# Performance work log

Measured on AMD Instinct MI355X. Metric: run time of the kernel, lower is better.

Reference implementation:

```python
import jax, jax.numpy as jnp
import numpy as np

BATCH = 16384
IN_F = 4096
OUT_F = 4096
CP_H = 4
CP_W = 4
CP_B = 4


def _cubic_interp_matrix(n_out: int, n_cp: int, a: float = -0.75) -> jnp.ndarray:
    """Dense (n_out, n_cp) matrix replicating torch bicubic interpolation
    (Keys cubic convolution, a=-0.75) along one axis with align_corners=True
    and border replication (index clamping)."""
    # source coordinate for each output index (align_corners=True)
    x = jnp.arange(n_out, dtype=jnp.float32) * ((n_cp - 1) / (n_out - 1))
    x0 = jnp.floor(x)
    t = x - x0                      # fractional offset in [0,1)
    x0i = x0.astype(jnp.int32)

    def cub_inner(s):   # |s| <= 1
        return ((a + 2.0) * s - (a + 3.0)) * s * s + 1.0

    def cub_outer(s):   # 1 < |s| < 2
        return ((a * s - 5.0 * a) * s + 8.0 * a) * s - 4.0 * a

    # weights for taps at offsets -1, 0, +1, +2
    ws = (cub_outer(t + 1.0), cub_inner(t), cub_inner(1.0 - t), cub_outer(2.0 - t))
    A = jnp.zeros((n_out, n_cp), dtype=jnp.float32)
    for k, w in enumerate(ws):
        idx = jnp.clip(x0i + (k - 1), 0, n_cp - 1)  # replicate border
        A = A + w[:, None] * jax.nn.one_hot(idx, n_cp, dtype=jnp.float32)
    return A


def _linear_interp_matrix(n_out: int, n_cp: int) -> jnp.ndarray:
    """Dense (n_out, n_cp) matrix replicating torch 1-D linear interpolation
    with align_corners=True."""
    x = jnp.arange(n_out, dtype=jnp.float32) * ((n_cp - 1) / (n_out - 1))
    lo = jnp.floor(x).astype(jnp.int32)
    t = x - lo.astype(jnp.float32)
    hi = jnp.clip(lo + 1, 0, n_cp - 1)
    oh = lambda i: jax.nn.one_hot(i, n_cp, dtype=jnp.float32)
    return (1.0 - t)[:, None] * oh(lo) + t[:, None] * oh(hi)


def setup_inputs() -> dict:
    key = jax.random.key(0)
    k1, k2, k3 = jax.random.split(key, 3)
    return {
        "x": jax.random.normal(k1, (BATCH, IN_F), dtype=jnp.float32),
        "weight_cp": jax.random.normal(k2, (CP_H, CP_W), dtype=jnp.float32) * 0.02,
        "bias_cp": jax.random.normal(k3, (CP_B,), dtype=jnp.float32) * 0.02,
    }


def reference(x, weight_cp, bias_cp):
    # Bicubic-interpolated dense weight: W = A_out @ CP @ A_in^T  (out, in)
    A_out = _cubic_interp_matrix(OUT_F, CP_H)
    A_in = _cubic_interp_matrix(IN_F, CP_W)
    W = A_out @ weight_cp @ A_in.T
    # Linearly interpolated bias (out,)
    bias = _linear_interp_matrix(OUT_F, CP_B) @ bias_cp
    # F.linear: y = x @ W^T + b
    return x @ W.T + bias
```

## Files before the change

kernel.cpp:

```cpp
#include <hip/hip_runtime.h>
#include <cstddef>

#define BATCH 16384
#define IN_F  4096
#define OUT_F 4096
#define ROWS_PER_BLOCK 64

__device__ __forceinline__ float cub_inner(float s) {
    return (1.25f * s - 2.25f) * s * s + 1.0f;
}
__device__ __forceinline__ float cub_outer(float s) {
    return ((-0.75f * s + 3.75f) * s - 6.0f) * s + 3.0f;
}

__device__ __forceinline__ void cubic_row(int i, float& a0, float& a1, float& a2, float& a3) {
    const float inv = 3.0f / 4095.0f;
    const float xi = (float)i * inv;
    const float x0 = floorf(xi);
    const float t  = xi - x0;
    const int   c  = (int)x0;
    const float w0 = cub_outer(t + 1.0f);
    const float w1 = cub_inner(t);
    const float w2 = cub_inner(1.0f - t);
    const float w3 = cub_outer(2.0f - t);
    if (c == 0)      { a0 = w0 + w1; a1 = w2;   a2 = w3;   a3 = 0.0f; }
    else if (c == 1) { a0 = w0;      a1 = w1;   a2 = w2;   a3 = w3; }
    else if (c == 2) { a0 = 0.0f;    a1 = w0;   a2 = w1;   a3 = w2 + w3; }
    else             { a0 = 0.0f;    a1 = 0.0f; a2 = w0;   a3 = w1 + w2 + w3; }
}

__global__ __launch_bounds__(256) void k_project(const float* __restrict__ x,
                                                 float* __restrict__ tproj) {
    const int b   = blockIdx.x;
    const int tid = threadIdx.x;
    const float4* xrow = (const float4*)(x + (size_t)b * IN_F);
    float acc0 = 0.f, acc1 = 0.f, acc2 = 0.f, acc3 = 0.f;
#pragma unroll
    for (int k = 0; k < 4; ++k) {
        const int v4 = k * 256 + tid;
        const float4 xv = xrow[v4];
        const int i = v4 * 4;
        float a0, a1, a2, a3;
        cubic_row(i + 0, a0, a1, a2, a3);
        acc0 += a0 * xv.x; acc1 += a1 * xv.x; acc2 += a2 * xv.x; acc3 += a3 * xv.x;
        cubic_row(i + 1, a0, a1, a2, a3);
        acc0 += a0 * xv.y; acc1 += a1 * xv.y; acc2 += a2 * xv.y; acc3 += a3 * xv.y;
        cubic_row(i + 2, a0, a1, a2, a3);
        acc0 += a0 * xv.z; acc1 += a1 * xv.z; acc2 += a2 * xv.z; acc3 += a3 * xv.z;
        cubic_row(i + 3, a0, a1, a2, a3);
        acc0 += a0 * xv.w; acc1 += a1 * xv.w; acc2 += a2 * xv.w; acc3 += a3 * xv.w;
    }
#pragma unroll
    for (int off = 32; off > 0; off >>= 1) {
        acc0 += __shfl_down(acc0, off);
        acc1 += __shfl_down(acc1, off);
        acc2 += __shfl_down(acc2, off);
        acc3 += __shfl_down(acc3, off);
    }
    __shared__ float lds[4][4];
    const int wid = tid >> 6;
    if ((tid & 63) == 0) {
        lds[wid][0] = acc0; lds[wid][1] = acc1; lds[wid][2] = acc2; lds[wid][3] = acc3;
    }
    __syncthreads();
    if (tid < 4) {
        tproj[(size_t)b * 4 + tid] = lds[0][tid] + lds[1][tid] + lds[2][tid] + lds[3][tid];
    }
}

__global__ __launch_bounds__(256) void k_expand(const float* __restrict__ tproj,
                                                const float* __restrict__ cp,
                                                const float* __restrict__ bcp,
                                                float* __restrict__ y) {
    const int oq = blockIdx.x * 256 + threadIdx.x;
    const int o0 = oq * 4;
    float cpr[16];
#pragma unroll
    for (int k = 0; k < 16; ++k) cpr[k] = cp[k];
    const float b0 = bcp[0], b1 = bcp[1], b2 = bcp[2], b3 = bcp[3];

    float we[4][4];
    float bs[4];
#pragma unroll
    for (int j = 0; j < 4; ++j) {
        const int o = o0 + j;
        float h0, h1, h2, h3;
        cubic_row(o, h0, h1, h2, h3);
#pragma unroll
        for (int w = 0; w < 4; ++w)
            we[j][w] = h0 * cpr[w] + h1 * cpr[4 + w] + h2 * cpr[8 + w] + h3 * cpr[12 + w];
        const float xb = (float)o * (3.0f / 4095.0f);
        const float lo = floorf(xb);
        const float tb = xb - lo;
        const int   l  = (int)lo;
        const float blo = (l == 0) ? b0 : (l == 1) ? b1 : (l == 2) ? b2 : b3;
        const float bhi = (l >= 2) ? b3 : (l == 1) ? b2 : b1;
        bs[j] = (1.0f - tb) * blo + tb * bhi;
    }

    const int r0 = blockIdx.y * ROWS_PER_BLOCK;
#pragma unroll 4
    for (int r = 0; r < ROWS_PER_BLOCK; ++r) {
        const int b = r0 + r;
        const float4 tv = *(const float4*)(tproj + (size_t)b * 4);
        float4 out;
        out.x = bs[0] + we[0][0]*tv.x + we[0][1]*tv.y + we[0][2]*tv.z + we[0][3]*tv.w;
        out.y = bs[1] + we[1][0]*tv.x + we[1][1]*tv.y + we[1][2]*tv.z + we[1][3]*tv.w;
        out.z = bs[2] + we[2][0]*tv.x + we[2][1]*tv.y + we[2][2]*tv.z + we[2][3]*tv.w;
        out.w = bs[3] + we[3][0]*tv.x + we[3][1]*tv.y + we[3][2]*tv.z + we[3][3]*tv.w;
        *(float4*)(y + (size_t)b * OUT_F + o0) = out;
    }
}

extern "C" void kernel_launch(void* const* d_in, const int* in_sizes, int n_in,
                              void* d_out, int out_size, void* d_ws, size_t ws_size,
                              hipStream_t stream) {
    const float* x   = (const float*)d_in[0];
    const float* cp  = (const float*)d_in[1];
    const float* bcp = (const float*)d_in[2];
    float* y = (float*)d_out;
    float* tproj = (float*)d_ws;

    k_project<<<dim3(BATCH), dim3(256), 0, stream>>>(x, tproj);
    dim3 g2(OUT_F / (256 * 4), BATCH / ROWS_PER_BLOCK);
    k_expand<<<g2, dim3(256), 0, stream>>>(tproj, cp, bcp, y);
}
```

Before: 484.9 us.

## Fuse projection and expansion into one kernel with precomputed interpolation tables

A small init kernel now precomputes the per-index cubic weights, the control-point-multiplied expansion weights and the interpolated bias into workspace tables. A single fused kernel then projects 16 rows of x to 4 values each, reduces them through LDS, and writes the corresponding output rows directly. This drops the separate tproj round trip and the per-element cubic weight evaluation in the hot loops. The cost is heavy register use for the preloaded tables and a block-level barrier between the read and write phases, which may limit overlap of loads and stores.

```diff
diff --git a/kernel.cpp b/kernel.cpp
--- a/kernel.cpp
+++ b/kernel.cpp
@@ -4,7 +4,8 @@
 #define BATCH 16384
 #define IN_F  4096
 #define OUT_F 4096
-#define ROWS_PER_BLOCK 64
+#define ROWS_PER_BLOCK 16
+#define NBLOCKS (BATCH / ROWS_PER_BLOCK)
 
 __device__ __forceinline__ float cub_inner(float s) {
     return (1.25f * s - 2.25f) * s * s + 1.0f;
@@ -29,86 +30,108 @@
     else             { a0 = 0.0f;    a1 = 0.0f; a2 = w0;   a3 = w1 + w2 + w3; }
 }
 
-__global__ __launch_bounds__(256) void k_project(const float* __restrict__ x,
-                                                 float* __restrict__ tproj) {
-    const int b   = blockIdx.x;
-    const int tid = threadIdx.x;
-    const float4* xrow = (const float4*)(x + (size_t)b * IN_F);
-    float acc0 = 0.f, acc1 = 0.f, acc2 = 0.f, acc3 = 0.f;
+__global__ __launch_bounds__(256) void k_init(const float* __restrict__ cp,
+                                              const float* __restrict__ bcp,
+                                              float4* __restrict__ Atab,
+                                              float4* __restrict__ Mtab,
+                                              float*  __restrict__ btab) {
+    const int i = blockIdx.x * 256 + threadIdx.x;
+    float a0, a1, a2, a3;
+    cubic_row(i, a0, a1, a2, a3);
+    Atab[i] = make_float4(a0, a1, a2, a3);
+
+    float4 m;
+    m.x = a0 * cp[0] + a1 * cp[4] + a2 * cp[8]  + a3 * cp[12];
+    m.y = a0 * cp[1] + a1 * cp[5] + a2 * cp[9]  + a3 * cp[13];
+    m.z = a0 * cp[2] + a1 * cp[6] + a2 * cp[10] + a3 * cp[14];
+    m.w = a0 * cp[3] + a1 * cp[7] + a2 * cp[11] + a3 * cp[15];
+    Mtab[i] = m;
+
+    const float xb = (float)i * (3.0f / 4095.0f);
+    const float lo = floorf(xb);
+    const float tb = xb - lo;
+    const int   l  = (int)lo;
+    const float b0 = bcp[0], b1 = bcp[1], b2 = bcp[2], b3 = bcp[3];
+    const float blo = (l == 0) ? b0 : (l == 1) ? b1 : (l == 2) ? b2 : b3;
+    const float bhi = (l >= 2) ? b3 : (l == 1) ? b2 : b1;
+    btab[i] = (1.0f - tb) * blo + tb * bhi;
+}
+
+__global__ __launch_bounds__(256) void k_fused(const float* __restrict__ x,
+                                               const float4* __restrict__ Atab,
+                                               const float4* __restrict__ Mtab,
+                                               const float4* __restrict__ btabv,
+                                               float* __restrict__ y) {
+    const int tid  = threadIdx.x;
+    const int wid  = tid >> 6;
+    const int lane = tid & 63;
+    const int row0 = blockIdx.x * ROWS_PER_BLOCK;
+
+    __shared__ float4 part[4][ROWS_PER_BLOCK];
+
+    float4 Af[16];
+#pragma unroll
+    for (int k = 0; k < 4; ++k)
+#pragma unroll
+        for (int j = 0; j < 4; ++j)
+            Af[k * 4 + j] = Atab[1024 * k + 4 * tid + j];
+
+#pragma unroll 2
+    for (int r = 0; r < ROWS_PER_BLOCK; ++r) {
+        const float4* xr = (const float4*)(x + (size_t)(row0 + r) * IN_F);
+        float s0 = 0.f, s1 = 0.f, s2 = 0.f, s3 = 0.f;
+#pragma unroll
+        for (int k = 0; k < 4; ++k) {
+            const float4 xv = xr[k * 256 + tid];
+            const float4 A0 = Af[k * 4 + 0], A1 = Af[k * 4 + 1];
+            const float4 A2 = Af[k * 4 + 2], A3 = Af[k * 4 + 3];
+            s0 += A0.x * xv.x + A1.x * xv.y + A2.x * xv.z + A3.x * xv.w;
+            s1 += A0.y * xv.x + A1.y * xv.y + A2.y * xv.z + A3.y * xv.w;
+            s2 += A0.z * xv.x + A1.z * xv.y + A2.z * xv.z + A3.z * xv.w;
+            s3 += A0.w * xv.x + A1.w * xv.y + A2.w * xv.z + A3.w * xv.w;
+        }
+#pragma unroll
+        for (int off = 32; off > 0; off >>= 1) {
+            s0 += __shfl_down(s0, off);
+            s1 += __shfl_down(s1, off);
+            s2 += __shfl_down(s2, off);
+            s3 += __shfl_down(s3, off);
+        }
+        if (lane == 0) part[wid][r] = make_float4(s0, s1, s2, s3);
+    }
+    __syncthreads();
+    __builtin_amdgcn_sched_barrier(0);
+
+    float4 Mf[16];
+    float4 bf[4];
 #pragma unroll
     for (int k = 0; k < 4; ++k) {
-        const int v4 = k * 256 + tid;
-        const float4 xv = xrow[v4];
-        const int i = v4 * 4;
-        float a0, a1, a2, a3;
-        cubic_row(i + 0, a0, a1, a2, a3);
-        acc0 += a0 * xv.x; acc1 += a1 * xv.x; acc2 += a2 * xv.x; acc3 += a3 * xv.x;
-        cubic_row(i + 1, a0, a1, a2, a3);
-        acc0 += a0 * xv.y; acc1 += a1 * xv.y; acc2 += a2 * xv.y; acc3 += a3 * xv.y;
-        cubic_row(i + 2, a0, a1, a2, a3);
-        acc0 += a0 * xv.z; acc1 += a1 * xv.z; acc2 += a2 * xv.z; acc3 += a3 * xv.z;
-        cubic_row(i + 3, a0, a1, a2, a3);
-        acc0 += a0 * xv.w; acc1 += a1 * xv.w; acc2 += a2 * xv.w; acc3 += a3 * xv.w;
-    }
 #pragma unroll
-    for (int off = 32; off > 0; off >>= 1) {
-        acc0 += __shfl_down(acc0, off);
-        acc1 += __shfl_down(acc1, off);
-        acc2 += __shfl_down(acc2, off);
-        acc3 += __shfl_down(acc3, off);
-    }
-    __shared__ float lds[4][4];
-    const int wid = tid >> 6;
-    if ((tid & 63) == 0) {
-        lds[wid][0] = acc0; lds[wid][1] = acc1; lds[wid][2] = acc2; lds[wid][3] = acc3;
-    }
-    __syncthreads();
-    if (tid < 4) {
-        tproj[(size_t)b * 4 + tid] = lds[0][tid] + lds[1][tid] + lds[2][tid] + lds[3][tid];
-    }
-}
-
-__global__ __launch_bounds__(256) void k_expand(const float* __restrict__ tproj,
-                                                const float* __restrict__ cp,
-                                                const float* __restrict__ bcp,
-                                                float* __restrict__ y) {
-    const int oq = blockIdx.x * 256 + threadIdx.x;
-    const int o0 = oq * 4;
-    float cpr[16];
-#pragma unroll
-    for (int k = 0; k < 16; ++k) cpr[k] = cp[k];
-    const float b0 = bcp[0], b1 = bcp[1], b2 = bcp[2], b3 = bcp[3];
-
-    float we[4][4];
-    float bs[4];
-#pragma unroll
-    for (int j = 0; j < 4; ++j) {
-        const int o = o0 + j;
-        float h0, h1, h2, h3;
-        cubic_row(o, h0, h1, h2, h3);
-#pragma unroll
-        for (int w = 0; w < 4; ++w)
-            we[j][w] = h0 * cpr[w] + h1 * cpr[4 + w] + h2 * cpr[8 + w] + h3 * cpr[12 + w];
-        const float xb = (float)o * (3.0f / 4095.0f);
-        const float lo = floorf(xb);
-        const float tb = xb - lo;
-        const int   l  = (int)lo;
-        const float blo = (l == 0) ? b0 : (l == 1) ? b1 : (l == 2) ? b2 : b3;
-        const float bhi = (l >= 2) ? b3 : (l == 1) ? b2 : b1;
-        bs[j] = (1.0f - tb) * blo + tb * bhi;
+        for (int j = 0; j < 4; ++j)
+            Mf[k * 4 + j] = Mtab[1024 * k + 4 * tid + j];
+        bf[k] = btabv[256 * k + tid];
     }
 
-    const int r0 = blockIdx.y * ROWS_PER_BLOCK;
-#pragma unroll 4
+#pragma unroll 2
     for (int r = 0; r < ROWS_PER_BLOCK; ++r) {
-        const int b = r0 + r;
-        const float4 tv = *(const float4*)(tproj + (size_t)b * 4);
-        float4 out;
-        out.x = bs[0] + we[0][0]*tv.x + we[0][1]*tv.y + we[0][2]*tv.z + we[0][3]*tv.w;
-        out.y = bs[1] + we[1][0]*tv.x + we[1][1]*tv.y + we[1][2]*tv.z + we[1][3]*tv.w;
-        out.z = bs[2] + we[2][0]*tv.x + we[2][1]*tv.y + we[2][2]*tv.z + we[2][3]*tv.w;
-        out.w = bs[3] + we[3][0]*tv.x + we[3][1]*tv.y + we[3][2]*tv.z + we[3][3]*tv.w;
-        *(float4*)(y + (size_t)b * OUT_F + o0) = out;
+        const float4 p0 = part[0][r], p1 = part[1][r], p2 = part[2][r], p3 = part[3][r];
+        float4 u;
+        u.x = (p0.x + p1.x) + (p2.x + p3.x);
+        u.y = (p0.y + p1.y) + (p2.y + p3.y);
+        u.z = (p0.z + p1.z) + (p2.z + p3.z);
+        u.w = (p0.w + p1.w) + (p2.w + p3.w);
+        float4* yr = (float4*)(y + (size_t)(row0 + r) * OUT_F);
+#pragma unroll
+        for (int k = 0; k < 4; ++k) {
+            const float4 M0 = Mf[k * 4 + 0], M1 = Mf[k * 4 + 1];
+            const float4 M2 = Mf[k * 4 + 2], M3 = Mf[k * 4 + 3];
+            float4 o;
+            o.x = bf[k].x + M0.x * u.x + M0.y * u.y + M0.z * u.z + M0.w * u.w;
+            o.y = bf[k].y + M1.x * u.x + M1.y * u.y + M1.z * u.z + M1.w * u.w;
+            o.z = bf[k].z + M2.x * u.x + M2.y * u.y + M2.z * u.z + M2.w * u.w;
+            o.w = bf[k].w + M3.x * u.x + M3.y * u.y + M3.z * u.z + M3.w * u.w;
+            yr[k * 256 + tid] = o;
+        }
     }
 }
 
@@ -119,9 +142,11 @@
     const float* cp  = (const float*)d_in[1];
     const float* bcp = (const float*)d_in[2];
     float* y = (float*)d_out;
-    float* tproj = (float*)d_ws;
 
-    k_project<<<dim3(BATCH), dim3(256), 0, stream>>>(x, tproj);
-    dim3 g2(OUT_F / (256 * 4), BATCH / ROWS_PER_BLOCK);
-    k_expand<<<g2, dim3(256), 0, stream>>>(tproj, cp, bcp, y);
+    float4* Atab = (float4*)d_ws;
+    float4* Mtab = (float4*)((char*)d_ws + 64 * 1024);
+    float*  btab = (float*)((char*)d_ws + 128 * 1024);
+
+    k_init<<<dim3(IN_F / 256), dim3(256), 0, stream>>>(cp, bcp, Atab, Mtab, btab);
+    k_fused<<<dim3(NBLOCKS), dim3(256), 0, stream>>>(x, Atab, Mtab, (const float4*)btab, y);
 }
```

Result: no change. 483.9 us (-0.2%).
